# Kernel tuning notes

Hardware: AMD Instinct MI355X
Metric: run time of the kernel (lower is better)

Reference implementation:

```python
import jax, jax.numpy as jnp
import numpy as np

N_NODES = 100000
N_EDGES = 1600000
IN_DIM = 128
HID = 64
NUM_GRAPHS = 2048
NUM_CLASSES = 1


def setup_inputs() -> dict:
    key = jax.random.key(0)
    ks = jax.random.split(key, 16)
    x = jax.random.normal(ks[0], (N_NODES, IN_DIM), dtype=jnp.float32)
    edge_index = jax.random.randint(ks[1], (2, N_EDGES), 0, N_NODES, dtype=jnp.int64)
    batch_index = jnp.sort(jax.random.randint(ks[2], (N_NODES,), 0, NUM_GRAPHS, dtype=jnp.int64))
    # GCNConv weights (glorot-ish scale)
    def lin(k, fi, fo):
        return jax.random.normal(k, (fi, fo), dtype=jnp.float32) / np.sqrt(fi)
    W1 = lin(ks[3], IN_DIM, HID); b1 = jnp.zeros((HID,), jnp.float32)
    W2 = lin(ks[4], HID, HID);    b2 = jnp.zeros((HID,), jnp.float32)
    W3 = lin(ks[5], HID, HID);    b3 = jnp.zeros((HID,), jnp.float32)
    W4 = lin(ks[6], HID, HID);    b4 = jnp.zeros((HID,), jnp.float32)
    Wout = lin(ks[7], 2 * HID, NUM_CLASSES); bout = jnp.zeros((NUM_CLASSES,), jnp.float32)
    return {"x": x, "edge_index": edge_index, "batch_index": batch_index,
            "W1": W1, "b1": b1, "W2": W2, "b2": b2, "W3": W3, "b3": b3,
            "W4": W4, "b4": b4, "Wout": Wout, "bout": bout}


def _gcn_conv(x, W, b, src, dst, norm, n):
    # PyG GCNConv: linear transform, then D^-1/2 (A+I) D^-1/2 aggregation, then bias
    h = x @ W                                   # [N, F_out]
    msg = h[src] * norm[:, None]                # [E+N, F_out] gather + scale
    agg = jax.ops.segment_sum(msg, dst, num_segments=n)
    return agg + b


def reference(x, edge_index, batch_index, W1, b1, W2, b2, W3, b3, W4, b4, Wout, bout):
    n = x.shape[0]
    loops = jnp.arange(n, dtype=edge_index.dtype)
    src = jnp.concatenate([edge_index[0], loops])  # add self-loops
    dst = jnp.concatenate([edge_index[1], loops])
    deg = jax.ops.segment_sum(jnp.ones_like(dst, dtype=x.dtype), dst, num_segments=n)
    dis = jax.lax.rsqrt(deg)                       # deg >= 1 due to self-loops
    norm = dis[src] * dis[dst]

    h = x
    for (W, b) in ((W1, b1), (W2, b2), (W3, b3), (W4, b4)):
        h = jax.nn.relu(_gcn_conv(h, W, b, src, dst, norm, n))

    # global mean pool + global max pool per graph
    counts = jax.ops.segment_sum(jnp.ones((n,), h.dtype), batch_index, num_segments=NUM_GRAPHS)
    mean = jax.ops.segment_sum(h, batch_index, num_segments=NUM_GRAPHS) / jnp.maximum(counts, 1.0)[:, None]
    mx = jax.ops.segment_max(h, batch_index, num_segments=NUM_GRAPHS)
    mx = jnp.where(counts[:, None] > 0, mx, 0.0)
    pooled = jnp.concatenate([mean, mx], axis=1)   # [G, 2*HID]

    out = pooled @ Wout + bout                     # [G, 1]
    return (out, pooled)
```

## Files before the change

kernel.cpp:

```cpp
#include <hip/hip_runtime.h>
#include <hip/hip_fp16.h>

#define N_NODES 100000
#define IN_DIM 128
#define HID 64
#define NUM_GRAPHS 2048
#define CNE_MAX (1600000 + 7 * N_NODES)
#define BROWS 128
#define NBUCK ((N_NODES + BROWS - 1) / BROWS)
#define NCHUNK 128
#define TOTP (NBUCK * NCHUNK)
#define CAP 4096

typedef _Float16 h8 __attribute__((ext_vector_type(8)));
typedef float f4 __attribute__((ext_vector_type(4)));


__global__ __launch_bounds__(256) void hist_partial(const int* __restrict__ dst,
                                                    int* __restrict__ partial,
                                                    int E, int chunk) {
    __shared__ int lh[NBUCK];
    int t = threadIdx.x, c = blockIdx.x;
    for (int b = t; b < NBUCK; b += 256) lh[b] = 0;
    __syncthreads();
    int lo = c * chunk, hi = min(lo + chunk, E);
    for (int i = lo + t; i < hi; i += 256) atomicAdd(&lh[dst[i] >> 7], 1);
    __syncthreads();
    for (int b = t; b < NBUCK; b += 256) partial[b * NCHUNK + c] = lh[b];
}

__global__ void scan1(const int* __restrict__ counts, int* __restrict__ out1,
                      int* __restrict__ bsum, int n, int pad8) {
    __shared__ int s[256];
    int t = threadIdx.x;
    int base = blockIdx.x * 1024 + t * 4;
    int v[4];
#pragma unroll
    for (int i = 0; i < 4; i++) {
        int c = (base + i < n) ? counts[base + i] : 0;
        v[i] = pad8 ? ((c + 7) & ~7) : c;
    }
    int tsum = v[0] + v[1] + v[2] + v[3];
    s[t] = tsum;
    __syncthreads();
    for (int off = 1; off < 256; off <<= 1) {
        int tv = (t >= off) ? s[t - off] : 0;
        __syncthreads();
        s[t] += tv;
        __syncthreads();
    }
    int excl = s[t] - tsum;
    if (t == 255) bsum[blockIdx.x] = s[255];
    int run = excl;
#pragma unroll
    for (int i = 0; i < 4; i++) {
        run += v[i];
        if (base + i < n) out1[base + i] = run;
    }
}

__global__ void scan2(const int* __restrict__ bsum, int* __restrict__ boff, int nb) {
    __shared__ int s[128];
    int t = threadIdx.x;
    int v = (t < nb) ? bsum[t] : 0;
    s[t] = v;
    __syncthreads();
    for (int off = 1; off < 128; off <<= 1) {
        int tv = (t >= off) ? s[t - off] : 0;
        __syncthreads();
        s[t] += tv;
        __syncthreads();
    }
    if (t < nb) boff[t] = s[t] - v;
}

__global__ void scan3(int* __restrict__ row_ptr, const int* __restrict__ boff, int n) {
    int i = blockIdx.x * blockDim.x + threadIdx.x;
    if (i == 0) row_ptr[0] = 0;
    if (i < n) row_ptr[i + 1] += boff[i >> 10];
}

__global__ void scan3p(const int* __restrict__ partial, const int* __restrict__ pincl,
                       const int* __restrict__ boff, int* __restrict__ base,
                       int* __restrict__ part_off, int E) {
    int i = blockIdx.x * blockDim.x + threadIdx.x;
    if (i < TOTP) {
        int v = pincl[i] + boff[i >> 10] - partial[i];
        base[i] = v;
        if ((i & (NCHUNK - 1)) == 0) part_off[i / NCHUNK] = v;
    }
    if (i == 0) part_off[NBUCK] = E;
}

__global__ __launch_bounds__(256) void partition_edges(const int* __restrict__ src,
                                                       const int* __restrict__ dst,
                                                       const int* __restrict__ base,
                                                       unsigned* __restrict__ part,
                                                       int E, int chunk) {
    __shared__ int cur[NBUCK];
    int t = threadIdx.x, c = blockIdx.x;
    for (int b = t; b < NBUCK; b += 256) cur[b] = base[b * NCHUNK + c];
    __syncthreads();
    int lo = c * chunk, hi = min(lo + chunk, E);
    for (int i = lo + t; i < hi; i += 256) {
        int s = src[i], d = dst[i];
        int pos = atomicAdd(&cur[d >> 7], 1);
        part[pos] = (unsigned)s | ((unsigned)(d & (BROWS - 1)) << 17);
    }
}

__global__ __launch_bounds__(256) void deg_dis(const unsigned* __restrict__ part,
                                               const int* __restrict__ part_off,
                                               int* __restrict__ pdeg,
                                               float* __restrict__ dis, int n) {
    __shared__ int cnt[BROWS];
    int t = threadIdx.x, b = blockIdx.x;
    int r0 = b * BROWS;
    if (t < BROWS) cnt[t] = 0;
    __syncthreads();
    for (int i = part_off[b] + t; i < part_off[b + 1]; i += 256)
        atomicAdd(&cnt[part[i] >> 17], 1);
    __syncthreads();
    int nrows = min(BROWS, n - r0);
    if (t < nrows) {
        int dg = cnt[t];
        pdeg[r0 + t] = dg;
        dis[r0 + t] = rsqrtf((float)(dg + 1));
    }
}

__global__ __launch_bounds__(256) void build_csr(const unsigned* __restrict__ part,
                                                 const int* __restrict__ part_off,
                                                 const int* __restrict__ row_ptr,
                                                 int* __restrict__ cne, int n) {
    __shared__ int fill[BROWS];
    __shared__ int stage[CAP];
    int b = blockIdx.x;
    int r0 = b * BROWS;
    int t = threadIdx.x;
    int nrows = min(BROWS, n - r0);
    int base = row_ptr[r0];
    int region = row_ptr[r0 + nrows] - base;
    for (int r = t; r < nrows; r += 256) fill[r] = row_ptr[r0 + r] - base;
    int i0 = part_off[b], i1 = part_off[b + 1];
    if (region <= CAP) {
        for (int i = t; i < region; i += 256) stage[i] = N_NODES;
        __syncthreads();
        for (int i = i0 + t; i < i1; i += 256) {
            unsigned pe = part[i];
            int pos = atomicAdd(&fill[pe >> 17], 1);
            stage[pos] = (int)(pe & 0x1FFFFu);
        }
        __syncthreads();
        for (int i = t; i < region; i += 256) cne[base + i] = stage[i];
    } else {
        for (int i = t; i < region; i += 256) cne[base + i] = N_NODES;
        __syncthreads();
        for (int i = i0 + t; i < i1; i += 256) {
            unsigned pe = part[i];
            int pos = atomicAdd(&fill[pe >> 17], 1);
            cne[base + pos] = (int)(pe & 0x1FFFFu);
        }
    }
}


template <int K, typename XT>
__global__ __launch_bounds__(256) void gemm_mfma(const XT* __restrict__ X,
                                                 const float* __restrict__ W,
                                                 const float* __restrict__ dis,
                                                 __half* __restrict__ out, int n) {
    const int KS = K / 32;
    int wave = threadIdx.x >> 6, lane = threadIdx.x & 63;
    int quad = lane >> 4, l16 = lane & 15;
    h8 b[4][KS];
#pragma unroll
    for (int ct = 0; ct < 4; ct++)
#pragma unroll
        for (int ks = 0; ks < KS; ks++)
#pragma unroll
            for (int j = 0; j < 8; j++)
                b[ct][ks][j] = (_Float16)W[(ks * 32 + quad * 8 + j) * HID + ct * 16 + l16];
    int ntile = n >> 4;
    int wpb = blockDim.x >> 6;
    int stride = gridDim.x * wpb;
    for (int rt = blockIdx.x * wpb + wave; rt < ntile; rt += stride) {
        int row0 = rt << 4;
        const XT* xr = X + (size_t)(row0 + l16) * K + quad * 8;
        f4 acc[4];
#pragma unroll
        for (int ct = 0; ct < 4; ct++) acc[ct] = (f4)(0.f);
#pragma unroll
        for (int ks = 0; ks < KS; ks++) {
            h8 a;
            if constexpr (__is_same(XT, float)) {
                float4 xa = *(const float4*)(xr + ks * 32);
                float4 xb = *(const float4*)(xr + ks * 32 + 4);
                a[0] = (_Float16)xa.x; a[1] = (_Float16)xa.y;
                a[2] = (_Float16)xa.z; a[3] = (_Float16)xa.w;
                a[4] = (_Float16)xb.x; a[5] = (_Float16)xb.y;
                a[6] = (_Float16)xb.z; a[7] = (_Float16)xb.w;
            } else {
                a = *(const h8*)(xr + ks * 32);
            }
#pragma unroll
            for (int ct = 0; ct < 4; ct++)
                acc[ct] = __builtin_amdgcn_mfma_f32_16x16x32_f16(a, b[ct][ks], acc[ct], 0, 0, 0);
        }
        int r0 = row0 + quad * 4;
        float4 dv = *(const float4*)(dis + r0);
        float dd[4] = {dv.x, dv.y, dv.z, dv.w};
#pragma unroll
        for (int reg = 0; reg < 4; reg++) {
            __half* orow = out + (size_t)(r0 + reg) * HID + l16;
            orow[0]  = __float2half(dd[reg] * acc[0][reg]);
            orow[16] = __float2half(dd[reg] * acc[1][reg]);
            orow[32] = __float2half(dd[reg] * acc[2][reg]);
            orow[48] = __float2half(dd[reg] * acc[3][reg]);
        }
    }
}

template <typename OutT>
__global__ __launch_bounds__(256) void aggregate(const __half* __restrict__ tmp,
                                                 const float* __restrict__ dis,
                                                 const int* __restrict__ row_ptr,
                                                 const int* __restrict__ cne,
                                                 const float* __restrict__ bias,
                                                 OutT* __restrict__ out, int n) {
    int wave = threadIdx.x >> 6, lane = threadIdx.x & 63;
    int wpb = blockDim.x >> 6;
    int stride = gridDim.x * wpb;
    float bl = bias[lane];
    for (int row = blockIdx.x * wpb + wave; row < n; row += stride) {
        float dr = dis[row];
        float a0 = __half2float(tmp[row * HID + lane]);
        float a1 = 0.f, a2 = 0.f, a3 = 0.f, a4 = 0.f, a5 = 0.f, a6 = 0.f, a7 = 0.f;
        int s = row_ptr[row], e = row_ptr[row + 1];
        if (s < e) {
            int4 ia0 = *(const int4*)(cne + s);
            int4 ia1 = *(const int4*)(cne + s + 4);
            float v0 = __half2float(tmp[ia0.x * HID + lane]);
            float v1 = __half2float(tmp[ia0.y * HID + lane]);
            float v2 = __half2float(tmp[ia0.z * HID + lane]);
            float v3 = __half2float(tmp[ia0.w * HID + lane]);
            float v4 = __half2float(tmp[ia1.x * HID + lane]);
            float v5 = __half2float(tmp[ia1.y * HID + lane]);
            float v6 = __half2float(tmp[ia1.z * HID + lane]);
            float v7 = __half2float(tmp[ia1.w * HID + lane]);
            int4 ib0, ib1;
            if (s + 8 < e) {
                ib0 = *(const int4*)(cne + s + 8);
                ib1 = *(const int4*)(cne + s + 12);
            }
            for (int t = s + 8; t < e; t += 8) {
                float u0 = __half2float(tmp[ib0.x * HID + lane]);
                float u1 = __half2float(tmp[ib0.y * HID + lane]);
                float u2 = __half2float(tmp[ib0.z * HID + lane]);
                float u3 = __half2float(tmp[ib0.w * HID + lane]);
                float u4 = __half2float(tmp[ib1.x * HID + lane]);
                float u5 = __half2float(tmp[ib1.y * HID + lane]);
                float u6 = __half2float(tmp[ib1.z * HID + lane]);
                float u7 = __half2float(tmp[ib1.w * HID + lane]);
                if (t + 8 < e) {
                    ib0 = *(const int4*)(cne + t + 8);
                    ib1 = *(const int4*)(cne + t + 12);
                }
                a0 += v0; a1 += v1; a2 += v2; a3 += v3;
                a4 += v4; a5 += v5; a6 += v6; a7 += v7;
                v0 = u0; v1 = u1; v2 = u2; v3 = u3;
                v4 = u4; v5 = u5; v6 = u6; v7 = u7;
            }
            a0 += v0; a1 += v1; a2 += v2; a3 += v3;
            a4 += v4; a5 += v5; a6 += v6; a7 += v7;
        }
        float r = dr * (((a0 + a1) + (a2 + a3)) + ((a4 + a5) + (a6 + a7))) + bl;
        r = fmaxf(r, 0.f);
        if constexpr (__is_same(OutT, __half))
            out[row * HID + lane] = __float2half(r);
        else
            out[row * HID + lane] = r;
    }
}

__global__ __launch_bounds__(256) void pool_kernel(const float* __restrict__ h,
                                                   const int* __restrict__ batch,
                                                   const float* __restrict__ Wout,
                                                   const float* __restrict__ bout,
                                                   float* __restrict__ d_out, int n) {
    __shared__ float ssum[4][64];
    __shared__ float smax[4][64];
    int g = blockIdx.x;
    int wave = threadIdx.x >> 6, j = threadIdx.x & 63;
    int lo = 0, hi = n;
    while (lo < hi) { int mid = (lo + hi) >> 1; if (batch[mid] < g) lo = mid + 1; else hi = mid; }
    int start = lo;
    hi = n;
    while (lo < hi) { int mid = (lo + hi) >> 1; if (batch[mid] < g + 1) lo = mid + 1; else hi = mid; }
    int end = lo;

    float sum = 0.f, mx = 0.f;
    for (int i = start + wave; i < end; i += 4) {
        float v = h[(size_t)i * HID + j];
        sum += v;
        mx = fmaxf(mx, v);
    }
    ssum[wave][j] = sum;
    smax[wave][j] = mx;
    __syncthreads();
    if (wave == 0) {
        sum = (ssum[0][j] + ssum[1][j]) + (ssum[2][j] + ssum[3][j]);
        mx = fmaxf(fmaxf(smax[0][j], smax[1][j]), fmaxf(smax[2][j], smax[3][j]));
        float cnt = (float)(end - start);
        float mean = sum / fmaxf(cnt, 1.f);
        float* pooled = d_out + NUM_GRAPHS;
        pooled[(size_t)g * (2 * HID) + j] = mean;
        pooled[(size_t)g * (2 * HID) + HID + j] = mx;
        float c = mean * Wout[j] + mx * Wout[HID + j];
#pragma unroll
        for (int off = 32; off; off >>= 1) c += __shfl_down(c, off);
        if (j == 0) d_out[g] = c + bout[0];
    }
}


extern "C" void kernel_launch(void* const* d_in, const int* in_sizes, int n_in,
                              void* d_out, int out_size, void* d_ws, size_t ws_size,
                              hipStream_t stream) {
    const float* x    = (const float*)d_in[0];
    const int*   edge = (const int*)d_in[1];
    const int*   batch= (const int*)d_in[2];
    const float* W1 = (const float*)d_in[3];  const float* b1 = (const float*)d_in[4];
    const float* W2 = (const float*)d_in[5];  const float* b2 = (const float*)d_in[6];
    const float* W3 = (const float*)d_in[7];  const float* b3 = (const float*)d_in[8];
    const float* W4 = (const float*)d_in[9];  const float* b4 = (const float*)d_in[10];
    const float* Wout = (const float*)d_in[11]; const float* bout = (const float*)d_in[12];
    float* out = (float*)d_out;

    const int N = N_NODES;
    const int E = in_sizes[1] / 2;
    const int* src = edge;
    const int* dst = edge + E;
    const int chunk = (E + NCHUNK - 1) / NCHUNK;

    char* p = (char*)d_ws;
    auto alloc = [&](size_t bytes) -> char* {
        char* r = p;
        p += (bytes + 255) & ~(size_t)255;
        return r;
    };
    int*      pdeg     = (int*)alloc((size_t)N * 4);
    int*      row_ptr  = (int*)alloc((size_t)(N + 1) * 4);
    int*      partial  = (int*)alloc((size_t)TOTP * 4);
    int*      pincl    = (int*)alloc((size_t)TOTP * 4);
    int*      pbase    = (int*)alloc((size_t)TOTP * 4);
    int*      part_off = (int*)alloc((size_t)(NBUCK + 1) * 4);
    unsigned* part     = (unsigned*)alloc((size_t)1600000 * 4);
    int*      cne      = (int*)alloc((size_t)CNE_MAX * 4);
    float*    dis      = (float*)alloc((size_t)N * 4);
    int*      bsum     = (int*)alloc(128 * 4);
    int*      boff     = (int*)alloc(128 * 4);
    __half*   tmp      = (__half*)alloc((size_t)(N + 1) * HID * 2);
    float*    hA       = (float*)alloc((size_t)N * HID * 4);
    __half*   hH       = (__half*)hA;

    hipMemsetAsync(tmp + (size_t)N * HID, 0, HID * 2, stream);

    hist_partial<<<NCHUNK, 256, 0, stream>>>(dst, partial, E, chunk);
    int nbp = (TOTP + 1023) / 1024;
    scan1<<<nbp, 256, 0, stream>>>(partial, pincl, bsum, TOTP, 0);
    scan2<<<1, 128, 0, stream>>>(bsum, boff, nbp);
    scan3p<<<(TOTP + 255) / 256, 256, 0, stream>>>(partial, pincl, boff, pbase, part_off, E);
    partition_edges<<<NCHUNK, 256, 0, stream>>>(src, dst, pbase, part, E, chunk);
    deg_dis<<<NBUCK, 256, 0, stream>>>(part, part_off, pdeg, dis, N);

    int nb = (N + 1023) / 1024;
    scan1<<<nb, 256, 0, stream>>>(pdeg, row_ptr + 1, bsum, N, 1);
    scan2<<<1, 128, 0, stream>>>(bsum, boff, nb);
    scan3<<<(N + 255) / 256, 256, 0, stream>>>(row_ptr, boff, N);
    build_csr<<<NBUCK, 256, 0, stream>>>(part, part_off, row_ptr, cne, N);

    const int AGG_BLOCKS = 2048;
    const int GEMM_BLOCKS = 1024;

    gemm_mfma<IN_DIM, float><<<GEMM_BLOCKS, 256, 0, stream>>>(x, W1, dis, tmp, N);
    aggregate<__half><<<AGG_BLOCKS, 256, 0, stream>>>(tmp, dis, row_ptr, cne, b1, hH, N);
    gemm_mfma<HID, _Float16><<<GEMM_BLOCKS, 256, 0, stream>>>((_Float16*)hH, W2, dis, tmp, N);
    aggregate<__half><<<AGG_BLOCKS, 256, 0, stream>>>(tmp, dis, row_ptr, cne, b2, hH, N);
    gemm_mfma<HID, _Float16><<<GEMM_BLOCKS, 256, 0, stream>>>((_Float16*)hH, W3, dis, tmp, N);
    aggregate<__half><<<AGG_BLOCKS, 256, 0, stream>>>(tmp, dis, row_ptr, cne, b3, hH, N);
    gemm_mfma<HID, _Float16><<<GEMM_BLOCKS, 256, 0, stream>>>((_Float16*)hH, W4, dis, tmp, N);
    aggregate<float><<<AGG_BLOCKS, 256, 0, stream>>>(tmp, dis, row_ptr, cne, b4, hA, N);

    pool_kernel<<<NUM_GRAPHS, 256, 0, stream>>>(hA, batch, Wout, bout, out, N);
}
```

Baseline: 397.1 us.

## Split waves into half-wave edge groups with half2 gathers in aggregation

The aggregate kernel now has each half of a wave gather a different neighbor row using 32-bit half2 loads, so one wave instruction covers two edges instead of one, and the two halves are combined with a cross-lane shuffle at the end. This is meant to cut the number of gather instructions and raise memory-level parallelism in the bandwidth-bound sparse aggregation. Only the low half-wave writes output. Separately, the edge partition chunk count is doubled to 256, so the histogram and partition kernels get more blocks, and the scan2 block size and its buffers are enlarged to match the larger partial count.

After: 377.9 us. -4.8%, faster.

```diff
diff --git a/kernel.cpp b/kernel.cpp
--- a/kernel.cpp
+++ b/kernel.cpp
@@ -8,7 +8,7 @@
 #define CNE_MAX (1600000 + 7 * N_NODES)
 #define BROWS 128
 #define NBUCK ((N_NODES + BROWS - 1) / BROWS)
-#define NCHUNK 128
+#define NCHUNK 256
 #define TOTP (NBUCK * NCHUNK)
 #define CAP 4096
 
@@ -60,12 +60,12 @@
 }
 
 __global__ void scan2(const int* __restrict__ bsum, int* __restrict__ boff, int nb) {
-    __shared__ int s[128];
+    __shared__ int s[256];
     int t = threadIdx.x;
     int v = (t < nb) ? bsum[t] : 0;
     s[t] = v;
     __syncthreads();
-    for (int off = 1; off < 128; off <<= 1) {
+    for (int off = 1; off < 256; off <<= 1) {
         int tv = (t >= off) ? s[t - off] : 0;
         __syncthreads();
         s[t] += tv;
@@ -229,57 +229,72 @@
                                                  const float* __restrict__ bias,
                                                  OutT* __restrict__ out, int n) {
     int wave = threadIdx.x >> 6, lane = threadIdx.x & 63;
+    int m = lane & 31, hh = lane >> 5;
     int wpb = blockDim.x >> 6;
     int stride = gridDim.x * wpb;
-    float bl = bias[lane];
+    float2 blv = *(const float2*)(bias + 2 * m);
     for (int row = blockIdx.x * wpb + wave; row < n; row += stride) {
         float dr = dis[row];
-        float a0 = __half2float(tmp[row * HID + lane]);
-        float a1 = 0.f, a2 = 0.f, a3 = 0.f, a4 = 0.f, a5 = 0.f, a6 = 0.f, a7 = 0.f;
+        float2 a0 = {0.f, 0.f}, a1 = {0.f, 0.f}, a2 = {0.f, 0.f}, a3 = {0.f, 0.f};
         int s = row_ptr[row], e = row_ptr[row + 1];
         if (s < e) {
-            int4 ia0 = *(const int4*)(cne + s);
-            int4 ia1 = *(const int4*)(cne + s + 4);
-            float v0 = __half2float(tmp[ia0.x * HID + lane]);
-            float v1 = __half2float(tmp[ia0.y * HID + lane]);
-            float v2 = __half2float(tmp[ia0.z * HID + lane]);
-            float v3 = __half2float(tmp[ia0.w * HID + lane]);
-            float v4 = __half2float(tmp[ia1.x * HID + lane]);
-            float v5 = __half2float(tmp[ia1.y * HID + lane]);
-            float v6 = __half2float(tmp[ia1.z * HID + lane]);
-            float v7 = __half2float(tmp[ia1.w * HID + lane]);
-            int4 ib0, ib1;
+            int4 i0 = *(const int4*)(cne + s);
+            int4 i1 = *(const int4*)(cne + s + 4);
+            int c0 = hh ? i0.y : i0.x;
+            int c1 = hh ? i0.w : i0.z;
+            int c2 = hh ? i1.y : i1.x;
+            int c3 = hh ? i1.w : i1.z;
+            __half2 g0 = *(const __half2*)(tmp + c0 * HID + 2 * m);
+            __half2 g1 = *(const __half2*)(tmp + c1 * HID + 2 * m);
+            __half2 g2 = *(const __half2*)(tmp + c2 * HID + 2 * m);
+            __half2 g3 = *(const __half2*)(tmp + c3 * HID + 2 * m);
+            int4 ni0, ni1;
             if (s + 8 < e) {
-                ib0 = *(const int4*)(cne + s + 8);
-                ib1 = *(const int4*)(cne + s + 12);
+                ni0 = *(const int4*)(cne + s + 8);
+                ni1 = *(const int4*)(cne + s + 12);
             }
             for (int t = s + 8; t < e; t += 8) {
-                float u0 = __half2float(tmp[ib0.x * HID + lane]);
-                float u1 = __half2float(tmp[ib0.y * HID + lane]);
-                float u2 = __half2float(tmp[ib0.z * HID + lane]);
-                float u3 = __half2float(tmp[ib0.w * HID + lane]);
-                float u4 = __half2float(tmp[ib1.x * HID + lane]);
-                float u5 = __half2float(tmp[ib1.y * HID + lane]);
-                float u6 = __half2float(tmp[ib1.z * HID + lane]);
-                float u7 = __half2float(tmp[ib1.w * HID + lane]);
+                int d0 = hh ? ni0.y : ni0.x;
+                int d1 = hh ? ni0.w : ni0.z;
+                int d2 = hh ? ni1.y : ni1.x;
+                int d3 = hh ? ni1.w : ni1.z;
+                __half2 u0 = *(const __half2*)(tmp + d0 * HID + 2 * m);
+                __half2 u1 = *(const __half2*)(tmp + d1 * HID + 2 * m);
+                __half2 u2 = *(const __half2*)(tmp + d2 * HID + 2 * m);
+                __half2 u3 = *(const __half2*)(tmp + d3 * HID + 2 * m);
                 if (t + 8 < e) {
-                    ib0 = *(const int4*)(cne + t + 8);
-                    ib1 = *(const int4*)(cne + t + 12);
+                    ni0 = *(const int4*)(cne + t + 8);
+                    ni1 = *(const int4*)(cne + t + 12);
                 }
-                a0 += v0; a1 += v1; a2 += v2; a3 += v3;
-                a4 += v4; a5 += v5; a6 += v6; a7 += v7;
-                v0 = u0; v1 = u1; v2 = u2; v3 = u3;
-                v4 = u4; v5 = u5; v6 = u6; v7 = u7;
+                float2 f0 = __half22float2(g0), f1 = __half22float2(g1);
+                float2 f2 = __half22float2(g2), f3 = __half22float2(g3);
+                a0.x += f0.x; a0.y += f0.y;
+                a1.x += f1.x; a1.y += f1.y;
+                a2.x += f2.x; a2.y += f2.y;
+                a3.x += f3.x; a3.y += f3.y;
+                g0 = u0; g1 = u1; g2 = u2; g3 = u3;
             }
-            a0 += v0; a1 += v1; a2 += v2; a3 += v3;
-            a4 += v4; a5 += v5; a6 += v6; a7 += v7;
-        }
-        float r = dr * (((a0 + a1) + (a2 + a3)) + ((a4 + a5) + (a6 + a7))) + bl;
-        r = fmaxf(r, 0.f);
-        if constexpr (__is_same(OutT, __half))
-            out[row * HID + lane] = __float2half(r);
-        else
-            out[row * HID + lane] = r;
+            float2 f0 = __half22float2(g0), f1 = __half22float2(g1);
+            float2 f2 = __half22float2(g2), f3 = __half22float2(g3);
+            a0.x += f0.x; a0.y += f0.y;
+            a1.x += f1.x; a1.y += f1.y;
+            a2.x += f2.x; a2.y += f2.y;
+            a3.x += f3.x; a3.y += f3.y;
+        }
+        float sx = (a0.x + a1.x) + (a2.x + a3.x);
+        float sy = (a0.y + a1.y) + (a2.y + a3.y);
+        sx += __shfl_xor(sx, 32);
+        sy += __shfl_xor(sy, 32);
+        float2 selff = __half22float2(*(const __half2*)(tmp + row * HID + 2 * m));
+        float rx = fmaxf(dr * (selff.x + sx) + blv.x, 0.f);
+        float ry = fmaxf(dr * (selff.y + sy) + blv.y, 0.f);
+        if (hh == 0) {
+            if constexpr (__is_same(OutT, __half)) {
+                *(__half2*)(out + row * HID + 2 * m) = __floats2half2_rn(rx, ry);
+            } else {
+                *(float2*)(out + row * HID + 2 * m) = make_float2(rx, ry);
+            }
+        }
     }
 }
 
@@ -358,8 +373,8 @@
     unsigned* part     = (unsigned*)alloc((size_t)1600000 * 4);
     int*      cne      = (int*)alloc((size_t)CNE_MAX * 4);
     float*    dis      = (float*)alloc((size_t)N * 4);
-    int*      bsum     = (int*)alloc(128 * 4);
-    int*      boff     = (int*)alloc(128 * 4);
+    int*      bsum     = (int*)alloc(256 * 4);
+    int*      boff     = (int*)alloc(256 * 4);
     __half*   tmp      = (__half*)alloc((size_t)(N + 1) * HID * 2);
     float*    hA       = (float*)alloc((size_t)N * HID * 4);
     __half*   hH       = (__half*)hA;
@@ -369,14 +384,14 @@
     hist_partial<<<NCHUNK, 256, 0, stream>>>(dst, partial, E, chunk);
     int nbp = (TOTP + 1023) / 1024;
     scan1<<<nbp, 256, 0, stream>>>(partial, pincl, bsum, TOTP, 0);
-    scan2<<<1, 128, 0, stream>>>(bsum, boff, nbp);
+    scan2<<<1, 256, 0, stream>>>(bsum, boff, nbp);
     scan3p<<<(TOTP + 255) / 256, 256, 0, stream>>>(partial, pincl, boff, pbase, part_off, E);
     partition_edges<<<NCHUNK, 256, 0, stream>>>(src, dst, pbase, part, E, chunk);
     deg_dis<<<NBUCK, 256, 0, stream>>>(part, part_off, pdeg, dis, N);
 
     int nb = (N + 1023) / 1024;
     scan1<<<nb, 256, 0, stream>>>(pdeg, row_ptr + 1, bsum, N, 1);
-    scan2<<<1, 128, 0, stream>>>(bsum, boff, nb);
+    scan2<<<1, 256, 0, stream>>>(bsum, boff, nb);
     scan3<<<(N + 255) / 256, 256, 0, stream>>>(row_ptr, boff, N);
     build_csr<<<NBUCK, 256, 0, stream>>>(part, part_off, row_ptr, cne, N);
 
```
